# Optimization experiments

Measured on AMD Instinct MI355X. Metric: run time of the kernel, lower is better.

The kernel has to match this reference:

```python
import jax, jax.numpy as jnp
import numpy as np

N_HEADS = 16
HEAD_DIM = 64
D_MODEL = N_HEADS * HEAD_DIM  # 1024


def setup_inputs() -> dict:
    key = jax.random.key(0)
    ks = jax.random.split(key, 6)
    B, S, D = 2, 2048, D_MODEL
    s = 0.02
    return {
        "hidden_states": jax.random.normal(ks[0], (B, S, D), jnp.float32),
        "position_bias": jax.random.normal(ks[1], (1, N_HEADS, S, S), jnp.float32),
        "Wq": jax.random.normal(ks[2], (D, D), jnp.float32) * s,
        "Wk": jax.random.normal(ks[3], (D, D), jnp.float32) * s,
        "Wv": jax.random.normal(ks[4], (D, D), jnp.float32) * s,
        "Wo": jax.random.normal(ks[5], (D, D), jnp.float32) * s,
    }


def reference(hidden_states, position_bias, Wq, Wk, Wv, Wo):
    B, S, D = hidden_states.shape

    def split_heads(x):  # [B,S,D] -> [B,H,S,hd]
        return x.reshape(B, S, N_HEADS, HEAD_DIM).transpose(0, 2, 1, 3)

    q = split_heads(hidden_states @ Wq)
    k = split_heads(hidden_states @ Wk)
    v = split_heads(hidden_states @ Wv)

    # T5 attention: NO 1/sqrt(d) scaling; additive relative-position bias.
    scores = jnp.einsum("bhqd,bhkd->bhqk", q, k) + position_bias
    attn = jax.nn.softmax(scores.astype(jnp.float32), axis=-1).astype(scores.dtype)
    ctx = jnp.einsum("bhqk,bhkd->bhqd", attn, v)
    ctx = ctx.transpose(0, 2, 1, 3).reshape(B, S, D)
    return ctx @ Wo
```

## Files before the change

### kernel.cpp

```cpp
#include <hip/hip_runtime.h>
#include <hip/hip_bf16.h>
#include <stdint.h>

typedef __bf16 bf16_t;
typedef __bf16 bf16x4 __attribute__((ext_vector_type(4)));
typedef __bf16 bf16x8 __attribute__((ext_vector_type(8)));
typedef float  f32x4  __attribute__((ext_vector_type(4)));

#define S_LEN 2048
#define NH    16
#define HD    64
#define DM    1024
#define BATCH 2
#define M_TOT (BATCH * S_LEN)
#define SM_SHIFT 18.0f

__device__ __forceinline__ void gload16(const void* g, void* l) {
    __builtin_amdgcn_global_load_lds(
        (const __attribute__((address_space(1))) unsigned int*)g,
        (__attribute__((address_space(3))) unsigned int*)l, 16, 0, 0);
}

__global__ void convert_h(const float* __restrict__ X, bf16_t* __restrict__ Y, int n) {
    int i = (blockIdx.x * 256 + threadIdx.x) * 4;
    if (i >= n) return;
    float4 v = *(const float4*)(X + i);
    union { bf16_t h[4]; uint2 u; } pk;
    pk.h[0] = (bf16_t)v.x; pk.h[1] = (bf16_t)v.y;
    pk.h[2] = (bf16_t)v.z; pk.h[3] = (bf16_t)v.w;
    *(uint2*)(Y + i) = pk.u;
}

__global__ void convert_transpose_w4(const float* __restrict__ W0, const float* __restrict__ W1,
                                     const float* __restrict__ W2, const float* __restrict__ W3,
                                     bf16_t* __restrict__ D0, bf16_t* __restrict__ D3) {
    __shared__ float tile[32][33];
    const int z = blockIdx.z;
    const float* W = z == 0 ? W0 : z == 1 ? W1 : z == 2 ? W2 : W3;
    bf16_t* Wt = z < 3 ? D0 + (size_t)z * DM * DM : D3;
    const int tid = threadIdx.x;
    const int tx = tid & 31, ty = tid >> 5;
    const int bx = blockIdx.x * 32, by = blockIdx.y * 32;
#pragma unroll
    for (int it = 0; it < 4; ++it)
        tile[ty + it * 8][tx] = W[(size_t)(by + ty + it * 8) * DM + bx + tx];
    __syncthreads();
#pragma unroll
    for (int it = 0; it < 4; ++it)
        Wt[(size_t)(bx + ty + it * 8) * DM + by + tx] = (bf16_t)tile[tx][ty + it * 8];
}

template<int BN, int EPI>
__global__ __launch_bounds__(256)
void gemm_glds(const bf16_t* __restrict__ A, const bf16_t* __restrict__ Bt,
               float* __restrict__ Cf, bf16_t* __restrict__ Qb, bf16_t* __restrict__ Kb,
               bf16_t* __restrict__ Vtb, int M, int N, int K)
{
    constexpr int WN = BN / 2;
    constexpr int NJ = WN / 16;
    constexpr int RB = BN / 32;
    __shared__ bf16_t smem[16640];
    bf16_t* At  = smem;
    bf16_t* Bts = smem + 8192;

    const int tid  = threadIdx.x;
    const int lane = tid & 63;
    const int wave = tid >> 6;
    const int lc = lane & 15;
    const int l4 = lane >> 4;
    const int wr = wave >> 1, wc = wave & 1;
    const int m0 = blockIdx.y * 128;
    const int n0 = blockIdx.x * BN;
    const int srow = tid >> 3;
    const int scol = (tid & 7) * 8;

    f32x4 acc[4][NJ] = {};

    for (int k0 = 0; k0 < K; k0 += 64) {
        __syncthreads();
#pragma unroll
        for (int ro = 0; ro < 4; ++ro)
            gload16(A + (size_t)(m0 + ro * 32 + srow) * K + k0 + scol,
                    At + ro * 2048 + wave * 512);
#pragma unroll
        for (int ro = 0; ro < RB; ++ro)
            gload16(Bt + (size_t)(n0 + ro * 32 + srow) * K + k0 + scol,
                    Bts + ro * 2048 + wave * 512);
        __syncthreads();

        bf16x8 af[2][4], bfr[2][NJ];
#pragma unroll
        for (int kk = 0; kk < 2; ++kk) {
#pragma unroll
            for (int i = 0; i < 4; ++i)
                af[kk][i] = *(const bf16x8*)(At + (wr * 64 + i * 16 + lc) * 64 + kk * 32 + l4 * 8);
#pragma unroll
            for (int j = 0; j < NJ; ++j)
                bfr[kk][j] = *(const bf16x8*)(Bts + (wc * WN + j * 16 + lc) * 64 + kk * 32 + l4 * 8);
        }
#pragma unroll
        for (int kk = 0; kk < 2; ++kk)
#pragma unroll
            for (int i = 0; i < 4; ++i)
#pragma unroll
                for (int j = 0; j < NJ; ++j)
                    acc[i][j] = __builtin_amdgcn_mfma_f32_16x16x32_bf16(af[kk][i], bfr[kk][j], acc[i][j], 0, 0, 0);
    }

    if (EPI == 1) {
#pragma unroll
        for (int i = 0; i < 4; ++i)
#pragma unroll
            for (int j = 0; j < NJ; ++j)
#pragma unroll
                for (int r = 0; r < 4; ++r) {
                    int m = m0 + wr * 64 + i * 16 + l4 * 4 + r;
                    int n = n0 + wc * WN + j * 16 + lc;
                    Cf[(size_t)m * N + n] = acc[i][j][r];
                }
    } else {
        const int sel = n0 >> 10;
        if (sel < 2) {
            bf16_t* Dst = sel == 0 ? Qb : Kb;
#pragma unroll
            for (int i = 0; i < 4; ++i)
#pragma unroll
                for (int j = 0; j < NJ; ++j)
#pragma unroll
                    for (int r = 0; r < 4; ++r) {
                        int m = m0 + wr * 64 + i * 16 + l4 * 4 + r;
                        int n = (n0 & 1023) + wc * WN + j * 16 + lc;
                        int b = m >> 11, s = m & 2047, h = n >> 6, d = n & 63;
                        Dst[(((size_t)(b * NH + h)) * S_LEN + s) * HD + d] = (bf16_t)acc[i][j][r];
                    }
        } else {
            __syncthreads();
            bf16_t* Ct = smem;
#pragma unroll
            for (int i = 0; i < 4; ++i)
#pragma unroll
                for (int j = 0; j < NJ; ++j)
#pragma unroll
                    for (int r = 0; r < 4; ++r) {
                        int ml = wr * 64 + i * 16 + l4 * 4 + r;
                        int nl = wc * WN + j * 16 + lc;
                        Ct[nl * 130 + ml] = (bf16_t)acc[i][j][r];
                    }
            __syncthreads();
            const int rr = tid >> 1, c0 = (tid & 1) * 64;
            const int nn = (n0 - 2048) + rr;
            const int hh = nn >> 6, dd = nn & 63;
            const int bb = m0 >> 11, s0 = m0 & 2047;
            bf16_t* dst = Vtb + (((size_t)(bb * NH + hh)) * HD + dd) * S_LEN + s0 + c0;
            const bf16_t* srcr = Ct + rr * 130 + c0;
#pragma unroll
            for (int u = 0; u < 8; ++u)
                *(uint4*)(dst + u * 8) = *(const uint4*)(srcr + u * 8);
        }
    }
}

__global__ __launch_bounds__(512, 1)
void attn_kernel(const bf16_t* __restrict__ Q, const bf16_t* __restrict__ Kin,
                 const bf16_t* __restrict__ Vt, const float* __restrict__ bias,
                 bf16_t* __restrict__ Ctx)
{
    const int tid  = threadIdx.x;
    const int lane = tid & 63;
    const int wave = tid >> 6;
    const int b    = wave >> 2;
    const int w    = wave & 3;
    const int lc = lane & 15;
    const int l4 = lane >> 4;

    const int f   = blockIdx.x;
    const int xcd = f & 7;
    const int kk_ = f >> 3;
    const int h   = xcd * 2 + (kk_ >> 4);
    const int qt  = kk_ & 15;
    const int qw  = qt * 128 + w * 32;

    __shared__ bf16_t Kt[2][2][64 * 64];
    __shared__ bf16_t Vs[2][2][64 * 64];
    __shared__ bf16_t Pt[8][32 * 68];
    bf16_t* Pw = Pt[wave];

    const bf16_t* Qg = Q + (size_t)(b * NH + h) * S_LEN * HD;
    const bf16_t* Kg[2]; const bf16_t* Vg[2];
#pragma unroll
    for (int bb = 0; bb < 2; ++bb) {
        Kg[bb] = Kin + (size_t)(bb * NH + h) * S_LEN * HD;
        Vg[bb] = Vt  + (size_t)(bb * NH + h) * HD * S_LEN;
    }
    const float* Bg = bias + (size_t)h * S_LEN * S_LEN;

    bf16x8 qf[2][2];
#pragma unroll
    for (int i = 0; i < 2; ++i)
#pragma unroll
        for (int kk = 0; kk < 2; ++kk)
            qf[i][kk] = *(const bf16x8*)(Qg + (size_t)(qw + i * 16 + lc) * HD + kk * 32 + l4 * 8);

    f32x4 cacc[2][4] = {};
    float lsum[2] = {};

    const int r0   = lane >> 3;
    const int gsrc = (lane & 7) ^ r0;
    const int R    = wave * 8;

    auto stage = [&](int t, int pbuf) {
        const int kv0 = t * 64;
        gload16(Kg[0] + (size_t)(kv0 + R + r0) * HD + gsrc * 8, &Kt[0][pbuf][R * 64]);
        gload16(Kg[1] + (size_t)(kv0 + R + r0) * HD + gsrc * 8, &Kt[1][pbuf][R * 64]);
        gload16(Vg[0] + (size_t)(R + r0) * S_LEN + kv0 + gsrc * 8, &Vs[0][pbuf][R * 64]);
        gload16(Vg[1] + (size_t)(R + r0) * S_LEN + kv0 + gsrc * 8, &Vs[1][pbuf][R * 64]);
    };

    auto loadbias = [&](int t, f32x4 (&bv)[2][4]) {
        const int kv0 = t * 64;
#pragma unroll
        for (int i = 0; i < 2; ++i)
#pragma unroll
            for (int j = 0; j < 4; ++j) {
                f32x4 v = *(const f32x4*)(Bg + (size_t)(qw + i * 16 + lc) * S_LEN + kv0 + j * 16 + l4 * 4);
                bv[i][j] = v - SM_SHIFT;
            }
    };

    auto round = [&](int t, f32x4 (&bcur)[2][4], f32x4 (&bnext)[2][4]) {
        const int buf = t & 1;
        if (t < 31) {
            stage(t + 1, buf ^ 1);
            loadbias(t + 1, bnext);
        }
        __builtin_amdgcn_sched_barrier(0);

        f32x4 saT[4][2] = {};
        __builtin_amdgcn_s_setprio(1);
#pragma unroll
        for (int kk = 0; kk < 2; ++kk) {
            bf16x8 kf[4];
#pragma unroll
            for (int j = 0; j < 4; ++j)
                kf[j] = *(const bf16x8*)(&Kt[b][buf][(j * 16 + lc) * 64 + (((kk * 4 + l4) ^ (lc & 7)) * 8)]);
#pragma unroll
            for (int j = 0; j < 4; ++j)
#pragma unroll
                for (int i = 0; i < 2; ++i)
                    saT[j][i] = __builtin_amdgcn_mfma_f32_16x16x32_bf16(kf[j], qf[i][kk], saT[j][i], 0, 0, 0);
        }
        __builtin_amdgcn_s_setprio(0);

#pragma unroll
        for (int i = 0; i < 2; ++i) {
#pragma unroll
            for (int j = 0; j < 4; ++j) {
                f32x4 s = saT[j][i] + bcur[i][j];
                float p0 = __expf(s.x), p1 = __expf(s.y), p2 = __expf(s.z), p3 = __expf(s.w);
                lsum[i] += (p0 + p1) + (p2 + p3);
                bf16x4 pk = {(bf16_t)p0, (bf16_t)p1, (bf16_t)p2, (bf16_t)p3};
                *(bf16x4*)(&Pw[(i * 16 + lc) * 68 + j * 16 + l4 * 4]) = pk;
            }
        }

        __builtin_amdgcn_s_setprio(1);
#pragma unroll
        for (int ks = 0; ks < 2; ++ks) {
            bf16x8 pf[2], vf[4];
#pragma unroll
            for (int i = 0; i < 2; ++i)
                pf[i] = *(const bf16x8*)(&Pw[(i * 16 + lc) * 68 + ks * 32 + l4 * 8]);
#pragma unroll
            for (int jd = 0; jd < 4; ++jd)
                vf[jd] = *(const bf16x8*)(&Vs[b][buf][(jd * 16 + lc) * 64 + (((ks * 4 + l4) ^ (lc & 7)) * 8)]);
#pragma unroll
            for (int i = 0; i < 2; ++i)
#pragma unroll
                for (int jd = 0; jd < 4; ++jd)
                    cacc[i][jd] = __builtin_amdgcn_mfma_f32_16x16x32_bf16(pf[i], vf[ks == 0 ? jd : jd], cacc[i][jd], 0, 0, 0),
                    (void)0;
#pragma unroll
            for (int i = 0; i < 2; ++i) (void)pf[i];
        }
        __builtin_amdgcn_s_setprio(0);
        __syncthreads();
    };

    f32x4 bvA[2][4], bvB[2][4];
    stage(0, 0);
    loadbias(0, bvA);
    __syncthreads();

    for (int ot = 0; ot < 16; ++ot) {
        round(2 * ot,     bvA, bvB);
        round(2 * ot + 1, bvB, bvA);
    }

#pragma unroll
    for (int i = 0; i < 2; ++i) {
        lsum[i] += __shfl_xor(lsum[i], 16, 64);
        lsum[i] += __shfl_xor(lsum[i], 32, 64);
    }
    float rinv[2][4];
#pragma unroll
    for (int i = 0; i < 2; ++i)
#pragma unroll
        for (int r = 0; r < 4; ++r)
            rinv[i][r] = 1.0f / __shfl(lsum[i], l4 * 4 + r, 16);

    bf16_t* Co = Ctx + (size_t)b * S_LEN * DM + (size_t)h * HD;
#pragma unroll
    for (int i = 0; i < 2; ++i)
#pragma unroll
        for (int r = 0; r < 4; ++r) {
            int qrow = qw + i * 16 + l4 * 4 + r;
#pragma unroll
            for (int jd = 0; jd < 4; ++jd)
                Co[(size_t)qrow * DM + jd * 16 + lc] = (bf16_t)(cacc[i][jd][r] * rinv[i][r]);
        }
}

extern "C" void kernel_launch(void* const* d_in, const int* in_sizes, int n_in,
                              void* d_out, int out_size, void* d_ws, size_t ws_size,
                              hipStream_t stream)
{
    (void)in_sizes; (void)n_in; (void)out_size; (void)ws_size;
    const float* hs   = (const float*)d_in[0];
    const float* bias = (const float*)d_in[1];
    const float* Wq   = (const float*)d_in[2];
    const float* Wk   = (const float*)d_in[3];
    const float* Wv   = (const float*)d_in[4];
    const float* Wo   = (const float*)d_in[5];
    float* out = (float*)d_out;

    char* ws = (char*)d_ws;
    bf16_t* Hbf   = (bf16_t*)(ws);
    bf16_t* Wqkvt = (bf16_t*)(ws + ( 8u << 20));
    bf16_t* Wot   = (bf16_t*)(ws + (14u << 20));
    bf16_t* Qb    = (bf16_t*)(ws + (16u << 20));
    bf16_t* Kb    = (bf16_t*)(ws + (24u << 20));
    bf16_t* Vtb   = (bf16_t*)(ws + (32u << 20));
    bf16_t* Ctx   = (bf16_t*)(ws + (40u << 20));

    convert_h<<<4096, 256, 0, stream>>>(hs, Hbf, M_TOT * DM);
    dim3 tg(32, 32, 4);
    convert_transpose_w4<<<tg, 256, 0, stream>>>(Wq, Wk, Wv, Wo, Wqkvt, Wot);

    dim3 gq(3 * DM / 128, M_TOT / 128);
    gemm_glds<128, 0><<<gq, 256, 0, stream>>>(Hbf, Wqkvt, nullptr, Qb, Kb, Vtb,
                                              M_TOT, 3 * DM, DM);

    attn_kernel<<<256, 512, 0, stream>>>(Qb, Kb, Vtb, bias, Ctx);

    dim3 go(DM / 64, M_TOT / 128);
    gemm_glds<64, 1><<<go, 256, 0, stream>>>(Ctx, Wot, out, nullptr, nullptr, nullptr,
                                             M_TOT, DM, DM);
}
```

Before: 220.3 us.

## Split attention blocks per batch instead of sharing bias across batches

```diff
diff --git a/kernel.cpp b/kernel.cpp
--- a/kernel.cpp
+++ b/kernel.cpp
@@ -160,7 +160,7 @@
     }
 }
 
-__global__ __launch_bounds__(512, 1)
+__global__ __launch_bounds__(256, 1)
 void attn_kernel(const bf16_t* __restrict__ Q, const bf16_t* __restrict__ Kin,
                  const bf16_t* __restrict__ Vt, const float* __restrict__ bias,
                  bf16_t* __restrict__ Ctx)
@@ -168,31 +168,27 @@
     const int tid  = threadIdx.x;
     const int lane = tid & 63;
     const int wave = tid >> 6;
-    const int b    = wave >> 2;
-    const int w    = wave & 3;
     const int lc = lane & 15;
     const int l4 = lane >> 4;
 
     const int f   = blockIdx.x;
-    const int xcd = f & 7;
-    const int kk_ = f >> 3;
+    const int b   = f >> 8;
+    const int g   = f & 255;
+    const int xcd = g & 7;
+    const int kk_ = g >> 3;
     const int h   = xcd * 2 + (kk_ >> 4);
     const int qt  = kk_ & 15;
-    const int qw  = qt * 128 + w * 32;
-
-    __shared__ bf16_t Kt[2][2][64 * 64];
-    __shared__ bf16_t Vs[2][2][64 * 64];
-    __shared__ bf16_t Pt[8][32 * 68];
+    const int qw  = qt * 128 + wave * 32;
+
+    __shared__ bf16_t Kt[2][64 * 64];
+    __shared__ bf16_t Vs[2][64 * 64];
+    __shared__ bf16_t Pt[4][32 * 68];
     bf16_t* Pw = Pt[wave];
 
-    const bf16_t* Qg = Q + (size_t)(b * NH + h) * S_LEN * HD;
-    const bf16_t* Kg[2]; const bf16_t* Vg[2];
-#pragma unroll
-    for (int bb = 0; bb < 2; ++bb) {
-        Kg[bb] = Kin + (size_t)(bb * NH + h) * S_LEN * HD;
-        Vg[bb] = Vt  + (size_t)(bb * NH + h) * HD * S_LEN;
-    }
-    const float* Bg = bias + (size_t)h * S_LEN * S_LEN;
+    const bf16_t* Qg = Q   + (size_t)(b * NH + h) * S_LEN * HD;
+    const bf16_t* Kg = Kin + (size_t)(b * NH + h) * S_LEN * HD;
+    const bf16_t* Vg = Vt  + (size_t)(b * NH + h) * HD * S_LEN;
+    const float*  Bg = bias + (size_t)h * S_LEN * S_LEN;
 
     bf16x8 qf[2][2];
 #pragma unroll
@@ -206,14 +202,14 @@
 
     const int r0   = lane >> 3;
     const int gsrc = (lane & 7) ^ r0;
-    const int R    = wave * 8;
+    const int R    = wave * 16;
 
     auto stage = [&](int t, int pbuf) {
         const int kv0 = t * 64;
-        gload16(Kg[0] + (size_t)(kv0 + R + r0) * HD + gsrc * 8, &Kt[0][pbuf][R * 64]);
-        gload16(Kg[1] + (size_t)(kv0 + R + r0) * HD + gsrc * 8, &Kt[1][pbuf][R * 64]);
-        gload16(Vg[0] + (size_t)(R + r0) * S_LEN + kv0 + gsrc * 8, &Vs[0][pbuf][R * 64]);
-        gload16(Vg[1] + (size_t)(R + r0) * S_LEN + kv0 + gsrc * 8, &Vs[1][pbuf][R * 64]);
+        gload16(Kg + (size_t)(kv0 + R + r0) * HD + gsrc * 8,     &Kt[pbuf][R * 64]);
+        gload16(Kg + (size_t)(kv0 + R + 8 + r0) * HD + gsrc * 8, &Kt[pbuf][(R + 8) * 64]);
+        gload16(Vg + (size_t)(R + r0) * S_LEN + kv0 + gsrc * 8,     &Vs[pbuf][R * 64]);
+        gload16(Vg + (size_t)(R + 8 + r0) * S_LEN + kv0 + gsrc * 8, &Vs[pbuf][(R + 8) * 64]);
     };
 
     auto loadbias = [&](int t, f32x4 (&bv)[2][4]) {
@@ -242,7 +238,7 @@
             bf16x8 kf[4];
 #pragma unroll
             for (int j = 0; j < 4; ++j)
-                kf[j] = *(const bf16x8*)(&Kt[b][buf][(j * 16 + lc) * 64 + (((kk * 4 + l4) ^ (lc & 7)) * 8)]);
+                kf[j] = *(const bf16x8*)(&Kt[buf][(j * 16 + lc) * 64 + (((kk * 4 + l4) ^ (lc & 7)) * 8)]);
 #pragma unroll
             for (int j = 0; j < 4; ++j)
 #pragma unroll
@@ -272,15 +268,12 @@
                 pf[i] = *(const bf16x8*)(&Pw[(i * 16 + lc) * 68 + ks * 32 + l4 * 8]);
 #pragma unroll
             for (int jd = 0; jd < 4; ++jd)
-                vf[jd] = *(const bf16x8*)(&Vs[b][buf][(jd * 16 + lc) * 64 + (((ks * 4 + l4) ^ (lc & 7)) * 8)]);
+                vf[jd] = *(const bf16x8*)(&Vs[buf][(jd * 16 + lc) * 64 + (((ks * 4 + l4) ^ (lc & 7)) * 8)]);
 #pragma unroll
             for (int i = 0; i < 2; ++i)
 #pragma unroll
                 for (int jd = 0; jd < 4; ++jd)
-                    cacc[i][jd] = __builtin_amdgcn_mfma_f32_16x16x32_bf16(pf[i], vf[ks == 0 ? jd : jd], cacc[i][jd], 0, 0, 0),
-                    (void)0;
-#pragma unroll
-            for (int i = 0; i < 2; ++i) (void)pf[i];
+                    cacc[i][jd] = __builtin_amdgcn_mfma_f32_16x16x32_bf16(pf[i], vf[jd], cacc[i][jd], 0, 0, 0);
         }
         __builtin_amdgcn_s_setprio(0);
         __syncthreads();
@@ -350,7 +343,7 @@
     gemm_glds<128, 0><<<gq, 256, 0, stream>>>(Hbf, Wqkvt, nullptr, Qb, Kb, Vtb,
                                               M_TOT, 3 * DM, DM);
 
-    attn_kernel<<<256, 512, 0, stream>>>(Qb, Kb, Vtb, bias, Ctx);
+    attn_kernel<<<512, 256, 0, stream>>>(Qb, Kb, Vtb, bias, Ctx);
 
     dim3 go(DM / 64, M_TOT / 128);
     gemm_glds<64, 1><<<go, 256, 0, stream>>>(Ctx, Wot, out, nullptr, nullptr, nullptr,
```

Result: slower. 252.7 us (+14.7%).
